# Kernel tuning notes

Hardware: AMD Instinct MI355X
Metric: run time of the kernel (lower is better)

The kernel has to match this reference:

```python
import jax, jax.numpy as jnp
import numpy as np

N_HID = 4
EPS = 1e-6  # LayerNorm eps (note: added to std, torch-style, std with ddof=1)


def _rnn_layer(wx_out, prev_pre, uh, g, b):
    """Sequential recurrence: at = wx_out[k] + h @ Uh^T; skip-subtract prev pre-act;
    custom layernorm (gamma*(x-mean)/(std+eps)+beta, std unbiased); relu.
    Returns (hiddens [T,B,H], pre_acts [T,B,H])."""
    T, B, H = wx_out.shape

    def step(h, inp):
        wx_k, prev_k = inp
        at = wx_k + h @ uh.T          # [B,H]
        pre = at
        a = at - prev_k               # skip connection (subtract prev layer pre-act)
        mean = a.mean(-1, keepdims=True)
        std = jnp.std(a, axis=-1, ddof=1, keepdims=True)
        a = g * (a - mean) / (std + EPS) + b
        h_new = jax.nn.relu(a)        # drop_mask = 1-drop_rate = 1.0 (test mode, drop_rate=0)
        return h_new, (h_new, pre)

    h0 = jnp.zeros((B, H), wx_out.dtype)
    _, (hs, pres) = jax.lax.scan(step, h0, (wx_out, prev_pre))
    return hs, pres


def setup_inputs() -> dict:
    key = jax.random.key(0)
    ks = jax.random.split(key, 12)
    T, B, D, H, C = 400, 32, 440, 1024, 3500
    s = 0.02
    return {
        "x": jax.random.normal(ks[0], (T, B, D), dtype=jnp.float32),
        "lab": jax.random.randint(ks[1], (T, B), 0, C),
        "test_flag": 1,
        "wx0_w": jax.random.normal(ks[2], (H, D), dtype=jnp.float32) * s,
        "wx0_b": jnp.zeros((H,), jnp.float32),
        "wx_w": jax.random.normal(ks[3], (N_HID - 1, H, H), dtype=jnp.float32) * s,
        "wx_b": jnp.zeros((N_HID - 1, H), jnp.float32),
        "uh_w": jax.random.normal(ks[4], (N_HID, H, H), dtype=jnp.float32) * s,
        "ln_g": jnp.ones((N_HID, H), jnp.float32),
        "ln_b": jnp.zeros((N_HID, H), jnp.float32),
        "fco_w": jax.random.normal(ks[5], (C, H), dtype=jnp.float32) * s,
        "fco_b": jnp.zeros((C,), jnp.float32),
    }


def reference(x, lab, test_flag, wx0_w, wx0_b, wx_w, wx_b, uh_w, ln_g, ln_b, fco_w, fco_b):
    T, B, _ = x.shape
    H = uh_w.shape[-1]
    prev_pre = jnp.zeros((T, B, H), x.dtype)  # skip_conn: layer 0 subtracts zeros
    h = x
    for i in range(N_HID):
        if i == 0:
            wx_out = jnp.einsum('tbd,hd->tbh', h, wx0_w) + wx0_b
        else:
            wx_out = jnp.einsum('tbd,hd->tbh', h, wx_w[i - 1]) + wx_b[i - 1]
        h, prev_pre = _rnn_layer(wx_out, prev_pre, uh_w[i], ln_g[i], ln_b[i])
    out = jnp.einsum('tbh,ch->tbc', h, fco_w) + fco_b   # [T,B,C]
    pout = jax.nn.log_softmax(out, axis=2)
    pred = jnp.argmax(pout, axis=2)
    nll = -jnp.take_along_axis(pout, lab[..., None], axis=2).squeeze(-1)
    loss = nll.mean()
    err = jnp.mean((pred != lab).astype(jnp.float32))
    return loss, err, pout
```

## Files before the change

kernel.cpp:

```cpp
#include <hip/hip_runtime.h>
#include <math.h>

#define T_STEPS 400
#define BATCH   32
#define HID     1024
#define MROWS   (T_STEPS * BATCH)
#define NCLS    3500
#define NG      8
#define BPG     4
#define CPG     32
#define JS      32
#define EPS     1e-6f
#define SLOTP   8

typedef __attribute__((ext_vector_type(8))) short short8v;
typedef __attribute__((ext_vector_type(4))) float f32x4;

__device__ __forceinline__ unsigned short bf16_rne(float x) {
  unsigned u = __builtin_bit_cast(unsigned, x);
  unsigned r = u + 0x7FFFu + ((u >> 16) & 1u);
  return (unsigned short)(r >> 16);
}

__device__ __forceinline__ unsigned pack_w(float x) {
  unsigned short h = bf16_rne(x);
  float fh = __builtin_bit_cast(float, (unsigned)h << 16);
  unsigned short l = bf16_rne(x - fh);
  return ((unsigned)h << 16) | (unsigned)l;
}
__device__ __forceinline__ float unpk_w(unsigned u) {
  float hi = __builtin_bit_cast(float, u & 0xFFFF0000u);
  float lo = __builtin_bit_cast(float, u << 16);
  return hi + lo;
}

__device__ __forceinline__ void stage_tile(
    const float* __restrict__ src, int rowlim, int row0, int ld,
    int k0, int K, unsigned short* hi, unsigned short* lo, int tid) {
  #pragma unroll
  for (int it = 0; it < 2; ++it) {
    const int task = tid + 256 * it;
    const int r = task >> 2, q = task & 3;
    const int gr = row0 + r;
    const bool rok = gr < rowlim;
    const float* p = src + (size_t)gr * ld + k0 + q * 8;
    float x[8];
    if (rok && (k0 + 32 <= K)) {
      float4 v0 = *(const float4*)p;
      float4 v1 = *(const float4*)(p + 4);
      x[0] = v0.x; x[1] = v0.y; x[2] = v0.z; x[3] = v0.w;
      x[4] = v1.x; x[5] = v1.y; x[6] = v1.z; x[7] = v1.w;
    } else {
      #pragma unroll
      for (int j = 0; j < 8; ++j)
        x[j] = (rok && (k0 + q * 8 + j) < K) ? p[j] : 0.f;
    }
    unsigned hp[4], lp[4];
    #pragma unroll
    for (int j = 0; j < 4; ++j) {
      unsigned short h0 = bf16_rne(x[2 * j]), h1 = bf16_rne(x[2 * j + 1]);
      float f0 = __builtin_bit_cast(float, (unsigned)h0 << 16);
      float f1 = __builtin_bit_cast(float, (unsigned)h1 << 16);
      unsigned short l0 = bf16_rne(x[2 * j] - f0), l1 = bf16_rne(x[2 * j + 1] - f1);
      hp[j] = (unsigned)h0 | ((unsigned)h1 << 16);
      lp[j] = (unsigned)l0 | ((unsigned)l1 << 16);
    }
    const int idx = (r * 4 + (q ^ (r & 3))) * 8;
    *(uint4*)&hi[idx] = make_uint4(hp[0], hp[1], hp[2], hp[3]);
    *(uint4*)&lo[idx] = make_uint4(lp[0], lp[1], lp[2], lp[3]);
  }
}

template <int NPASS>
__global__ __launch_bounds__(256) void gemm_mfma(
    const float* __restrict__ A, const float* __restrict__ W,
    const float* __restrict__ bias, float* __restrict__ C,
    int M, int N, int K) {
  __shared__ unsigned short Ah[128 * 32], Al[128 * 32];
  __shared__ unsigned short Bh[128 * 32], Bl[128 * 32];
  const int tid = threadIdx.x;
  const int m0 = blockIdx.y * 128, n0 = blockIdx.x * 128;
  const int w = tid >> 6, lane = tid & 63;
  const int rlow = lane & 15, ksel = lane >> 4;

  f32x4 acc[8][2];
  #pragma unroll
  for (int i = 0; i < 8; ++i) {
    acc[i][0] = (f32x4)(0.f);
    acc[i][1] = (f32x4)(0.f);
  }

  for (int k0 = 0; k0 < K; k0 += 32) {
    __syncthreads();
    stage_tile(A, M, m0, K, k0, K, Ah, Al, tid);
    stage_tile(W, N, n0, K, k0, K, Bh, Bl, tid);
    __syncthreads();

    short8v wh[2], wl[2];
    #pragma unroll
    for (int nf = 0; nf < 2; ++nf) {
      const int rn = w * 32 + nf * 16 + rlow;
      const int idx = (rn * 4 + (ksel ^ (rn & 3))) * 8;
      wh[nf] = *(const short8v*)&Bh[idx];
      if (NPASS == 3) wl[nf] = *(const short8v*)&Bl[idx];
    }
    #pragma unroll
    for (int i = 0; i < 8; ++i) {
      const int ra = i * 16 + rlow;
      const int idx = (ra * 4 + (ksel ^ (ra & 3))) * 8;
      short8v ah = *(const short8v*)&Ah[idx];
      if (NPASS == 3) {
        short8v al = *(const short8v*)&Al[idx];
        acc[i][0] = __builtin_amdgcn_mfma_f32_16x16x32_bf16(ah, wh[0], acc[i][0], 0, 0, 0);
        acc[i][0] = __builtin_amdgcn_mfma_f32_16x16x32_bf16(al, wh[0], acc[i][0], 0, 0, 0);
        acc[i][0] = __builtin_amdgcn_mfma_f32_16x16x32_bf16(ah, wl[0], acc[i][0], 0, 0, 0);
        acc[i][1] = __builtin_amdgcn_mfma_f32_16x16x32_bf16(ah, wh[1], acc[i][1], 0, 0, 0);
        acc[i][1] = __builtin_amdgcn_mfma_f32_16x16x32_bf16(al, wh[1], acc[i][1], 0, 0, 0);
        acc[i][1] = __builtin_amdgcn_mfma_f32_16x16x32_bf16(ah, wl[1], acc[i][1], 0, 0, 0);
      } else {
        acc[i][0] = __builtin_amdgcn_mfma_f32_16x16x32_bf16(ah, wh[0], acc[i][0], 0, 0, 0);
        acc[i][1] = __builtin_amdgcn_mfma_f32_16x16x32_bf16(ah, wh[1], acc[i][1], 0, 0, 0);
      }
    }
  }

  int col[2]; float bb[2]; bool cok[2];
  #pragma unroll
  for (int nf = 0; nf < 2; ++nf) {
    col[nf] = n0 + w * 32 + nf * 16 + rlow;
    cok[nf] = col[nf] < N;
    bb[nf] = cok[nf] ? bias[col[nf]] : 0.f;
  }
  #pragma unroll
  for (int i = 0; i < 8; ++i) {
    const int row = m0 + i * 16 + ksel * 4;
    #pragma unroll
    for (int nf = 0; nf < 2; ++nf) {
      if (cok[nf]) {
        float* cp = C + (size_t)row * N + col[nf];
        cp[0 * N] = acc[i][nf][0] + bb[nf];
        cp[1 * N] = acc[i][nf][1] + bb[nf];
        cp[2 * N] = acc[i][nf][2] + bb[nf];
        cp[3 * N] = acc[i][nf][3] + bb[nf];
      }
    }
  }
}

__global__ __launch_bounds__(256, 1) void scan_pair(
    const float* __restrict__ wx,
    const float* __restrict__ ua_w,
    const float* __restrict__ ub_w,
    const float* __restrict__ wb_w,
    const float* __restrict__ wb_bias,
    float* __restrict__ h_all,
    float* __restrict__ pre_prev,
    float* __restrict__ pre_out,
    float* __restrict__ a_pub,
    int* __restrict__ prog,
    const float* __restrict__ g_a, const float* __restrict__ be_a,
    const float* __restrict__ g_b, const float* __restrict__ be_b,
    int skip_sub) {
  const int tid  = threadIdx.x;
  const int g    = blockIdx.x >> 5;
  const int c    = blockIdx.x & 31;
  const int lane = tid & 63;
  const int wv   = tid >> 6;
  const int jw   = tid & 3;
  const int ks   = tid >> 2;
  const int col0 = c * JS + jw * 8;

  int* prog_g = prog + (size_t)g * CPG * SLOTP;

  __shared__ float h_a_lds[HID * BPG];
  __shared__ float h_b_lds[HID * BPG];
  __shared__ float a_lds[BPG * HID];
  __shared__ float partial_a[4][BPG][JS];
  __shared__ float partial_b[4][BPG][JS];
  __shared__ float stats_lds[BPG][2];

  float4 ua0[16], ua1[16], ub0[16], ub1[16];
  uint4  wp0[16], wp1[16];
  #pragma unroll
  for (int i = 0; i < 16; ++i) {
    const int kk = ks + 64 * i;
    float a0[8], b0[8], w0[8];
    #pragma unroll
    for (int q = 0; q < 8; ++q) {
      const size_t off = (size_t)(col0 + q) * HID + kk;
      a0[q] = ua_w[off];
      b0[q] = ub_w[off];
      w0[q] = wb_w[off];
    }
    ua0[i] = make_float4(a0[0], a0[1], a0[2], a0[3]);
    ua1[i] = make_float4(a0[4], a0[5], a0[6], a0[7]);
    ub0[i] = make_float4(b0[0], b0[1], b0[2], b0[3]);
    ub1[i] = make_float4(b0[4], b0[5], b0[6], b0[7]);
    wp0[i] = make_uint4(pack_w(w0[0]), pack_w(w0[1]), pack_w(w0[2]), pack_w(w0[3]));
    wp1[i] = make_uint4(pack_w(w0[4]), pack_w(w0[5]), pack_w(w0[6]), pack_w(w0[7]));
  }
  float ga[4], ba[4], gb[4], bb[4];
  #pragma unroll
  for (int j = 0; j < 4; ++j) {
    const int kk = tid + 256 * j;
    ga[j] = g_a[kk]; ba[j] = be_a[kk];
    gb[j] = g_b[kk]; bb[j] = be_b[kk];
  }
  float biasb = 0.f;
  if (tid < 128) biasb = wb_bias[c * JS + (tid & 31)];

  float wxa_r = 0.f, prev_r = 0.f, pre_a_reg = 0.f;
  if (tid < 128) {
    const size_t gi = ((size_t)0 * BATCH + g * BPG + (tid >> 5)) * HID + c * JS + (tid & 31);
    wxa_r = wx[gi];
    if (!skip_sub)
      prev_r = __hip_atomic_load(&pre_prev[gi], __ATOMIC_RELAXED, __HIP_MEMORY_SCOPE_AGENT);
  }
  __syncthreads();

  for (int k = 0; k <= T_STEPS; ++k) {
    const int par = k & 1;
    float* pa = a_pub + ((size_t)(par * 2 + 0) * NG + g) * (BPG * HID);
    float* pb = a_pub + ((size_t)(par * 2 + 1) * NG + g) * (BPG * HID);
    const bool doA = (k < T_STEPS);
    const bool doB = (k >= 1);

    if (doA && k > 0) {
      float pacc[4][8];
      #pragma unroll
      for (int b = 0; b < 4; ++b)
        #pragma unroll
        for (int q = 0; q < 8; ++q) pacc[b][q] = 0.f;
      #pragma unroll
      for (int i = 0; i < 16; ++i) {
        float4 h4 = *(const float4*)&h_a_lds[(ks + 64 * i) * 4];
        #pragma unroll
        for (int b = 0; b < 4; ++b) {
          float hb = ((const float*)&h4)[b];
          pacc[b][0] += hb * ua0[i].x; pacc[b][1] += hb * ua0[i].y;
          pacc[b][2] += hb * ua0[i].z; pacc[b][3] += hb * ua0[i].w;
          pacc[b][4] += hb * ua1[i].x; pacc[b][5] += hb * ua1[i].y;
          pacc[b][6] += hb * ua1[i].z; pacc[b][7] += hb * ua1[i].w;
        }
      }
      #pragma unroll
      for (int b = 0; b < 4; ++b)
        #pragma unroll
        for (int q = 0; q < 8; ++q) {
          float v = pacc[b][q];
          v += __shfl_xor(v, 4); v += __shfl_xor(v, 8);
          v += __shfl_xor(v, 16); v += __shfl_xor(v, 32);
          pacc[b][q] = v;
        }
      if ((lane >> 2) == 0) {
        #pragma unroll
        for (int b = 0; b < 4; ++b) {
          *(float4*)&partial_a[wv][b][jw * 8]     = *(const float4*)&pacc[b][0];
          *(float4*)&partial_a[wv][b][jw * 8 + 4] = *(const float4*)&pacc[b][4];
        }
      }
    }

    if (doB) {
      float pacc[4][8];
      #pragma unroll
      for (int b = 0; b < 4; ++b)
        #pragma unroll
        for (int q = 0; q < 8; ++q) pacc[b][q] = 0.f;
      #pragma unroll
      for (int i = 0; i < 16; ++i) {
        float4 ha = *(const float4*)&h_a_lds[(ks + 64 * i) * 4];
        float w[8];
        w[0] = unpk_w(wp0[i].x); w[1] = unpk_w(wp0[i].y);
        w[2] = unpk_w(wp0[i].z); w[3] = unpk_w(wp0[i].w);
        w[4] = unpk_w(wp1[i].x); w[5] = unpk_w(wp1[i].y);
        w[6] = unpk_w(wp1[i].z); w[7] = unpk_w(wp1[i].w);
        #pragma unroll
        for (int b = 0; b < 4; ++b) {
          float hv = ((const float*)&ha)[b];
          #pragma unroll
          for (int q = 0; q < 8; ++q) pacc[b][q] += hv * w[q];
        }
        if (k >= 2) {
          float4 hb4 = *(const float4*)&h_b_lds[(ks + 64 * i) * 4];
          #pragma unroll
          for (int b = 0; b < 4; ++b) {
            float hv = ((const float*)&hb4)[b];
            pacc[b][0] += hv * ub0[i].x; pacc[b][1] += hv * ub0[i].y;
            pacc[b][2] += hv * ub0[i].z; pacc[b][3] += hv * ub0[i].w;
            pacc[b][4] += hv * ub1[i].x; pacc[b][5] += hv * ub1[i].y;
            pacc[b][6] += hv * ub1[i].z; pacc[b][7] += hv * ub1[i].w;
          }
        }
      }
      #pragma unroll
      for (int b = 0; b < 4; ++b)
        #pragma unroll
        for (int q = 0; q < 8; ++q) {
          float v = pacc[b][q];
          v += __shfl_xor(v, 4); v += __shfl_xor(v, 8);
          v += __shfl_xor(v, 16); v += __shfl_xor(v, 32);
          pacc[b][q] = v;
        }
      if ((lane >> 2) == 0) {
        #pragma unroll
        for (int b = 0; b < 4; ++b) {
          *(float4*)&partial_b[wv][b][jw * 8]     = *(const float4*)&pacc[b][0];
          *(float4*)&partial_b[wv][b][jw * 8 + 4] = *(const float4*)&pacc[b][4];
        }
      }
    }
    __syncthreads();

    if (tid < 128) {
      const int b = tid >> 5, j = tid & 31;
      float at_a_new = 0.f;
      if (doA) {
        float red = 0.f;
        if (k > 0)
          red = partial_a[0][b][j] + partial_a[1][b][j]
              + partial_a[2][b][j] + partial_a[3][b][j];
        at_a_new = wxa_r + red;
        __hip_atomic_store(&pa[(size_t)b * HID + c * JS + j], at_a_new - prev_r,
                           __ATOMIC_RELAXED, __HIP_MEMORY_SCOPE_AGENT);
      }
      if (doB) {
        float redb = partial_b[0][b][j] + partial_b[1][b][j]
                   + partial_b[2][b][j] + partial_b[3][b][j];
        float at_b = biasb + redb;
        const size_t gib = ((size_t)(k - 1) * BATCH + g * BPG + b) * HID + c * JS + j;
        __hip_atomic_store(&pre_out[gib], at_b,
                           __ATOMIC_RELAXED, __HIP_MEMORY_SCOPE_AGENT);
        __hip_atomic_store(&pb[(size_t)b * HID + c * JS + j], at_b - pre_a_reg,
                           __ATOMIC_RELAXED, __HIP_MEMORY_SCOPE_AGENT);
      }
      if (doA) pre_a_reg = at_a_new;
    }
    asm volatile("s_waitcnt vmcnt(0)" ::: "memory");
    __syncthreads();

    if (tid == 0)
      __hip_atomic_store(&prog_g[c * SLOTP], k + 1,
                         __ATOMIC_RELAXED, __HIP_MEMORY_SCOPE_AGENT);

    float wxa_n = 0.f, prev_n = 0.f;
    if (k + 1 < T_STEPS && tid < 128) {
      const size_t gi = ((size_t)(k + 1) * BATCH + g * BPG + (tid >> 5)) * HID
                        + c * JS + (tid & 31);
      wxa_n = wx[gi];
      if (!skip_sub)
        prev_n = __hip_atomic_load(&pre_prev[gi], __ATOMIC_RELAXED, __HIP_MEMORY_SCOPE_AGENT);
    }

    {
      const int* p = &prog_g[(lane & 31) * SLOTP];
      while (true) {
        int v = __hip_atomic_load(p, __ATOMIC_RELAXED, __HIP_MEMORY_SCOPE_AGENT);
        if (__all(v >= k + 1)) break;
        __builtin_amdgcn_s_sleep(1);
      }
    }

    float ta[16], tb[16];
    if (doA) {
      #pragma unroll
      for (int j = 0; j < 16; ++j)
        ta[j] = __hip_atomic_load(&pa[tid + 256 * j],
                                  __ATOMIC_RELAXED, __HIP_MEMORY_SCOPE_AGENT);
    }
    if (doB) {
      #pragma unroll
      for (int j = 0; j < 16; ++j)
        tb[j] = __hip_atomic_load(&pb[tid + 256 * j],
                                  __ATOMIC_RELAXED, __HIP_MEMORY_SCOPE_AGENT);
    }

    if (doA) {
      #pragma unroll
      for (int j = 0; j < 16; ++j) a_lds[tid + 256 * j] = ta[j];
      __syncthreads();
      {
        float s1 = 0.f, s2 = 0.f;
        #pragma unroll
        for (int i = 0; i < 16; ++i) {
          float v = a_lds[wv * HID + i * 64 + lane];
          s1 += v; s2 += v * v;
        }
        #pragma unroll
        for (int m = 1; m <= 32; m <<= 1) { s1 += __shfl_xor(s1, m); s2 += __shfl_xor(s2, m); }
        if (lane == 0) {
          float mean = s1 * (1.f / HID);
          float var = (s2 - (float)HID * mean * mean) * (1.f / (float)(HID - 1));
          stats_lds[wv][0] = mean;
          stats_lds[wv][1] = sqrtf(fmaxf(var, 0.f)) + EPS;
        }
      }
      __syncthreads();
      {
        float m0 = stats_lds[0][0], r0 = 1.f / stats_lds[0][1];
        float m1 = stats_lds[1][0], r1 = 1.f / stats_lds[1][1];
        float m2 = stats_lds[2][0], r2 = 1.f / stats_lds[2][1];
        float m3 = stats_lds[3][0], r3 = 1.f / stats_lds[3][1];
        #pragma unroll
        for (int j = 0; j < 4; ++j) {
          const int kk = tid + 256 * j;
          float h0 = fmaxf(ga[j] * (a_lds[0 * HID + kk] - m0) * r0 + ba[j], 0.f);
          float h1 = fmaxf(ga[j] * (a_lds[1 * HID + kk] - m1) * r1 + ba[j], 0.f);
          float h2 = fmaxf(ga[j] * (a_lds[2 * HID + kk] - m2) * r2 + ba[j], 0.f);
          float h3 = fmaxf(ga[j] * (a_lds[3 * HID + kk] - m3) * r3 + ba[j], 0.f);
          *(float4*)&h_a_lds[kk * 4] = make_float4(h0, h1, h2, h3);
        }
      }
      __syncthreads();
    }

    if (doB) {
      #pragma unroll
      for (int j = 0; j < 16; ++j) a_lds[tid + 256 * j] = tb[j];
      __syncthreads();
      {
        float s1 = 0.f, s2 = 0.f;
        #pragma unroll
        for (int i = 0; i < 16; ++i) {
          float v = a_lds[wv * HID + i * 64 + lane];
          s1 += v; s2 += v * v;
        }
        #pragma unroll
        for (int m = 1; m <= 32; m <<= 1) { s1 += __shfl_xor(s1, m); s2 += __shfl_xor(s2, m); }
        if (lane == 0) {
          float mean = s1 * (1.f / HID);
          float var = (s2 - (float)HID * mean * mean) * (1.f / (float)(HID - 1));
          stats_lds[wv][0] = mean;
          stats_lds[wv][1] = sqrtf(fmaxf(var, 0.f)) + EPS;
        }
      }
      __syncthreads();
      {
        float m0 = stats_lds[0][0], r0 = 1.f / stats_lds[0][1];
        float m1 = stats_lds[1][0], r1 = 1.f / stats_lds[1][1];
        float m2 = stats_lds[2][0], r2 = 1.f / stats_lds[2][1];
        float m3 = stats_lds[3][0], r3 = 1.f / stats_lds[3][1];
        #pragma unroll
        for (int j = 0; j < 4; ++j) {
          const int kk = tid + 256 * j;
          float h0 = fmaxf(gb[j] * (a_lds[0 * HID + kk] - m0) * r0 + bb[j], 0.f);
          float h1 = fmaxf(gb[j] * (a_lds[1 * HID + kk] - m1) * r1 + bb[j], 0.f);
          float h2 = fmaxf(gb[j] * (a_lds[2 * HID + kk] - m2) * r2 + bb[j], 0.f);
          float h3 = fmaxf(gb[j] * (a_lds[3 * HID + kk] - m3) * r3 + bb[j], 0.f);
          *(float4*)&h_b_lds[kk * 4] = make_float4(h0, h1, h2, h3);
          if (c == 0) {
            const size_t hb0 = ((size_t)(k - 1) * BATCH + g * BPG) * HID + kk;
            h_all[hb0 + 0 * HID] = h0;
            h_all[hb0 + 1 * HID] = h1;
            h_all[hb0 + 2 * HID] = h2;
            h_all[hb0 + 3 * HID] = h3;
          }
        }
      }
    }
    __syncthreads();

    wxa_r = wxa_n; prev_r = prev_n;
  }
}

__global__ __launch_bounds__(256) void softmax_loss(
    float* __restrict__ out, const int* __restrict__ lab, float* __restrict__ acc) {
  __shared__ float rowbuf[NCLS];
  __shared__ float rv[4]; __shared__ int ri[4]; __shared__ float rs[4];
  __shared__ float shv[2];
  __shared__ int shidx;
  const int m = blockIdx.x;
  float* row = out + (size_t)m * NCLS;
  const int tid = threadIdx.x;
  const int lane = tid & 63, wid = tid >> 6;

  float vmax = -1e30f; int vidx = 0x7fffffff;
  for (int c2 = tid; c2 < NCLS / 2; c2 += 256) {
    float2 v = *(const float2*)(row + 2 * c2);
    rowbuf[2 * c2] = v.x; rowbuf[2 * c2 + 1] = v.y;
    if (v.x > vmax) { vmax = v.x; vidx = 2 * c2; }
    if (v.y > vmax) { vmax = v.y; vidx = (v.x > v.y) ? vidx : 2 * c2 + 1; }
  }
  #pragma unroll
  for (int off = 32; off; off >>= 1) {
    float ov = __shfl_down(vmax, off);
    int oi = __shfl_down(vidx, off);
    if (ov > vmax || (ov == vmax && oi < vidx)) { vmax = ov; vidx = oi; }
  }
  if (lane == 0) { rv[wid] = vmax; ri[wid] = vidx; }
  __syncthreads();
  if (tid == 0) {
    float bm = rv[0]; int bi = ri[0];
    for (int w = 1; w < 4; ++w)
      if (rv[w] > bm || (rv[w] == bm && ri[w] < bi)) { bm = rv[w]; bi = ri[w]; }
    shv[0] = bm; shidx = bi;
  }
  __syncthreads();
  float gmax = shv[0];
  float s = 0.f;
  for (int c = tid; c < NCLS; c += 256) s += expf(rowbuf[c] - gmax);
  #pragma unroll
  for (int off = 32; off; off >>= 1) s += __shfl_down(s, off);
  if (lane == 0) rs[wid] = s;
  __syncthreads();
  if (tid == 0) shv[1] = rs[0] + rs[1] + rs[2] + rs[3];
  __syncthreads();
  float lse = logf(shv[1]);
  for (int c2 = tid; c2 < NCLS / 2; c2 += 256) {
    float2 v;
    v.x = rowbuf[2 * c2] - gmax - lse;
    v.y = rowbuf[2 * c2 + 1] - gmax - lse;
    *(float2*)(row + 2 * c2) = v;
  }
  if (tid == 0) {
    int lb = lab[m];
    float nll = -(rowbuf[lb] - gmax - lse);
    atomicAdd(acc + 0, nll);
    atomicAdd(acc + 1, (shidx != lb) ? 1.f : 0.f);
  }
}

__global__ void init_acc(float* acc) { acc[threadIdx.x] = 0.f; }

__global__ void finalize_out(const float* __restrict__ acc, float* __restrict__ out) {
  out[0] = acc[0] * (1.f / (float)MROWS);
  out[1] = acc[1] * (1.f / (float)MROWS);
}

extern "C" void kernel_launch(void* const* d_in, const int* in_sizes, int n_in,
                              void* d_out, int out_size, void* d_ws, size_t ws_size,
                              hipStream_t stream) {
  const float* x     = (const float*)d_in[0];
  const int*   lab   = (const int*)d_in[1];
  const float* wx0_w = (const float*)d_in[3];
  const float* wx0_b = (const float*)d_in[4];
  const float* wx_w  = (const float*)d_in[5];
  const float* wx_b  = (const float*)d_in[6];
  const float* uh_w  = (const float*)d_in[7];
  const float* ln_g  = (const float*)d_in[8];
  const float* ln_b  = (const float*)d_in[9];
  const float* fco_w = (const float*)d_in[10];
  const float* fco_b = (const float*)d_in[11];
  float* out = (float*)d_out;

  float* wsf = (float*)d_ws;
  size_t off = 0;
  auto carve = [&](size_t n) { float* p = wsf + off; off += (n + 63) & ~(size_t)63; return p; };
  float* wxbuf = carve((size_t)MROWS * HID);
  float* h_all = carve((size_t)MROWS * HID);
  float* pre   = carve((size_t)MROWS * HID);
  float* a_pub = carve((size_t)2 * 2 * NG * BPG * HID);
  int*   prog  = (int*)carve((size_t)2 * NG * CPG * SLOTP);
  float* acc   = carve(64);

  (void)hipMemsetAsync(prog, 0, (size_t)2 * NG * CPG * SLOTP * sizeof(int), stream);
  init_acc<<<1, 2, 0, stream>>>(acc);

  const size_t HH = (size_t)HID * HID;

  gemm_mfma<3><<<dim3(HID / 128, MROWS / 128), 256, 0, stream>>>(
      x, wx0_w, wx0_b, wxbuf, MROWS, HID, 440);
  scan_pair<<<dim3(NG * CPG), 256, 0, stream>>>(
      wxbuf, uh_w + 0 * HH, uh_w + 1 * HH, wx_w + 0 * HH, wx_b + 0 * HID,
      h_all, pre , pre, a_pub, prog,
      ln_g + 0 * HID, ln_b + 0 * HID, ln_g + 1 * HID, ln_b + 1 * HID, 1);

  gemm_mfma<3><<<dim3(HID / 128, MROWS / 128), 256, 0, stream>>>(
      h_all, wx_w + 1 * HH, wx_b + 1 * HID, wxbuf, MROWS, HID, HID);
  scan_pair<<<dim3(NG * CPG), 256, 0, stream>>>(
      wxbuf, uh_w + 2 * HH, uh_w + 3 * HH, wx_w + 2 * HH, wx_b + 2 * HID,
      h_all, pre , pre, a_pub, prog + (size_t)NG * CPG * SLOTP,
      ln_g + 2 * HID, ln_b + 2 * HID, ln_g + 3 * HID, ln_b + 3 * HID, 0);

  gemm_mfma<1><<<dim3((NCLS + 127) / 128, MROWS / 128), 256, 0, stream>>>(
      h_all, fco_w, fco_b, out + 2, MROWS, NCLS, HID);
  softmax_loss<<<MROWS, 256, 0, stream>>>(out + 2, lab, acc);
  finalize_out<<<1, 1, 0, stream>>>(acc, out);
}
```

Measured before the change: 11.08 ms.

## Double scan block threads and process both layer normalizations concurrently

Raises the persistent scan kernel from 256 to 512 threads per block, splitting each K-reduction over 8 waves with 8 slices per thread. This frees enough registers to hold the inter-layer weight in plain fp32 instead of packed bf16 hi/lo pairs. It also merges the two per-step layernorm phases (layer A and layer B) into one pass where each half of the block handles one layer, which removes several barriers per timestep. The cost is more partial sums to reduce across waves, a larger shared-memory footprint, and a layout change to the published activation buffer.

Result: slower. 16.52 ms (+49.0%).

```diff
diff --git a/kernel.cpp b/kernel.cpp
--- a/kernel.cpp
+++ b/kernel.cpp
@@ -20,18 +20,6 @@
   unsigned u = __builtin_bit_cast(unsigned, x);
   unsigned r = u + 0x7FFFu + ((u >> 16) & 1u);
   return (unsigned short)(r >> 16);
-}
-
-__device__ __forceinline__ unsigned pack_w(float x) {
-  unsigned short h = bf16_rne(x);
-  float fh = __builtin_bit_cast(float, (unsigned)h << 16);
-  unsigned short l = bf16_rne(x - fh);
-  return ((unsigned)h << 16) | (unsigned)l;
-}
-__device__ __forceinline__ float unpk_w(unsigned u) {
-  float hi = __builtin_bit_cast(float, u & 0xFFFF0000u);
-  float lo = __builtin_bit_cast(float, u << 16);
-  return hi + lo;
 }
 
 __device__ __forceinline__ void stage_tile(
@@ -147,7 +135,7 @@
   }
 }
 
-__global__ __launch_bounds__(256, 1) void scan_pair(
+__global__ __launch_bounds__(512, 1) void scan_pair(
     const float* __restrict__ wx,
     const float* __restrict__ ua_w,
     const float* __restrict__ ub_w,
@@ -174,16 +162,15 @@
 
   __shared__ float h_a_lds[HID * BPG];
   __shared__ float h_b_lds[HID * BPG];
-  __shared__ float a_lds[BPG * HID];
-  __shared__ float partial_a[4][BPG][JS];
-  __shared__ float partial_b[4][BPG][JS];
-  __shared__ float stats_lds[BPG][2];
-
-  float4 ua0[16], ua1[16], ub0[16], ub1[16];
-  uint4  wp0[16], wp1[16];
-  #pragma unroll
-  for (int i = 0; i < 16; ++i) {
-    const int kk = ks + 64 * i;
+  __shared__ float a2_lds[2 * BPG * HID];
+  __shared__ float partial_a[8][BPG][JS];
+  __shared__ float partial_b[8][BPG][JS];
+  __shared__ float stats_lds[8][2];
+
+  float4 ua0[8], ua1[8], ub0[8], ub1[8], wb0[8], wb1[8];
+  #pragma unroll
+  for (int i = 0; i < 8; ++i) {
+    const int kk = ks + 128 * i;
     float a0[8], b0[8], w0[8];
     #pragma unroll
     for (int q = 0; q < 8; ++q) {
@@ -196,15 +183,16 @@
     ua1[i] = make_float4(a0[4], a0[5], a0[6], a0[7]);
     ub0[i] = make_float4(b0[0], b0[1], b0[2], b0[3]);
     ub1[i] = make_float4(b0[4], b0[5], b0[6], b0[7]);
-    wp0[i] = make_uint4(pack_w(w0[0]), pack_w(w0[1]), pack_w(w0[2]), pack_w(w0[3]));
-    wp1[i] = make_uint4(pack_w(w0[4]), pack_w(w0[5]), pack_w(w0[6]), pack_w(w0[7]));
-  }
-  float ga[4], ba[4], gb[4], bb[4];
+    wb0[i] = make_float4(w0[0], w0[1], w0[2], w0[3]);
+    wb1[i] = make_float4(w0[4], w0[5], w0[6], w0[7]);
+  }
+  const int half = tid >> 8, t2 = tid & 255;
+  float gq[4], bq[4];
   #pragma unroll
   for (int j = 0; j < 4; ++j) {
-    const int kk = tid + 256 * j;
-    ga[j] = g_a[kk]; ba[j] = be_a[kk];
-    gb[j] = g_b[kk]; bb[j] = be_b[kk];
+    const int kk = t2 + 256 * j;
+    gq[j] = half ? g_b[kk] : g_a[kk];
+    bq[j] = half ? be_b[kk] : be_a[kk];
   }
   float biasb = 0.f;
   if (tid < 128) biasb = wb_bias[c * JS + (tid & 31)];
@@ -220,8 +208,7 @@
 
   for (int k = 0; k <= T_STEPS; ++k) {
     const int par = k & 1;
-    float* pa = a_pub + ((size_t)(par * 2 + 0) * NG + g) * (BPG * HID);
-    float* pb = a_pub + ((size_t)(par * 2 + 1) * NG + g) * (BPG * HID);
+    float* pbase = a_pub + ((size_t)par * NG + g) * (2 * BPG * HID);
     const bool doA = (k < T_STEPS);
     const bool doB = (k >= 1);
 
@@ -232,8 +219,8 @@
         #pragma unroll
         for (int q = 0; q < 8; ++q) pacc[b][q] = 0.f;
       #pragma unroll
-      for (int i = 0; i < 16; ++i) {
-        float4 h4 = *(const float4*)&h_a_lds[(ks + 64 * i) * 4];
+      for (int i = 0; i < 8; ++i) {
+        float4 h4 = *(const float4*)&h_a_lds[(ks + 128 * i) * 4];
         #pragma unroll
         for (int b = 0; b < 4; ++b) {
           float hb = ((const float*)&h4)[b];
@@ -268,21 +255,18 @@
         #pragma unroll
         for (int q = 0; q < 8; ++q) pacc[b][q] = 0.f;
       #pragma unroll
-      for (int i = 0; i < 16; ++i) {
-        float4 ha = *(const float4*)&h_a_lds[(ks + 64 * i) * 4];
-        float w[8];
-        w[0] = unpk_w(wp0[i].x); w[1] = unpk_w(wp0[i].y);
-        w[2] = unpk_w(wp0[i].z); w[3] = unpk_w(wp0[i].w);
-        w[4] = unpk_w(wp1[i].x); w[5] = unpk_w(wp1[i].y);
-        w[6] = unpk_w(wp1[i].z); w[7] = unpk_w(wp1[i].w);
+      for (int i = 0; i < 8; ++i) {
+        float4 ha = *(const float4*)&h_a_lds[(ks + 128 * i) * 4];
         #pragma unroll
         for (int b = 0; b < 4; ++b) {
           float hv = ((const float*)&ha)[b];
-          #pragma unroll
-          for (int q = 0; q < 8; ++q) pacc[b][q] += hv * w[q];
+          pacc[b][0] += hv * wb0[i].x; pacc[b][1] += hv * wb0[i].y;
+          pacc[b][2] += hv * wb0[i].z; pacc[b][3] += hv * wb0[i].w;
+          pacc[b][4] += hv * wb1[i].x; pacc[b][5] += hv * wb1[i].y;
+          pacc[b][6] += hv * wb1[i].z; pacc[b][7] += hv * wb1[i].w;
         }
         if (k >= 2) {
-          float4 hb4 = *(const float4*)&h_b_lds[(ks + 64 * i) * 4];
+          float4 hb4 = *(const float4*)&h_b_lds[(ks + 128 * i) * 4];
           #pragma unroll
           for (int b = 0; b < 4; ++b) {
             float hv = ((const float*)&hb4)[b];
@@ -317,21 +301,24 @@
       float at_a_new = 0.f;
       if (doA) {
         float red = 0.f;
-        if (k > 0)
-          red = partial_a[0][b][j] + partial_a[1][b][j]
-              + partial_a[2][b][j] + partial_a[3][b][j];
+        if (k > 0) {
+          #pragma unroll
+          for (int w = 0; w < 8; ++w) red += partial_a[w][b][j];
+        }
         at_a_new = wxa_r + red;
-        __hip_atomic_store(&pa[(size_t)b * HID + c * JS + j], at_a_new - prev_r,
+        __hip_atomic_store(&pbase[(size_t)b * HID + c * JS + j], at_a_new - prev_r,
                            __ATOMIC_RELAXED, __HIP_MEMORY_SCOPE_AGENT);
       }
       if (doB) {
-        float redb = partial_b[0][b][j] + partial_b[1][b][j]
-                   + partial_b[2][b][j] + partial_b[3][b][j];
+        float redb = 0.f;
+        #pragma unroll
+        for (int w = 0; w < 8; ++w) redb += partial_b[w][b][j];
         float at_b = biasb + redb;
         const size_t gib = ((size_t)(k - 1) * BATCH + g * BPG + b) * HID + c * JS + j;
         __hip_atomic_store(&pre_out[gib], at_b,
                            __ATOMIC_RELAXED, __HIP_MEMORY_SCOPE_AGENT);
-        __hip_atomic_store(&pb[(size_t)b * HID + c * JS + j], at_b - pre_a_reg,
+        __hip_atomic_store(&pbase[(size_t)(BPG * HID) + b * HID + c * JS + j],
+                           at_b - pre_a_reg,
                            __ATOMIC_RELAXED, __HIP_MEMORY_SCOPE_AGENT);
       }
       if (doA) pre_a_reg = at_a_new;
@@ -361,100 +348,56 @@
       }
     }
 
-    float ta[16], tb[16];
-    if (doA) {
-      #pragma unroll
-      for (int j = 0; j < 16; ++j)
-        ta[j] = __hip_atomic_load(&pa[tid + 256 * j],
-                                  __ATOMIC_RELAXED, __HIP_MEMORY_SCOPE_AGENT);
-    }
-    if (doB) {
-      #pragma unroll
-      for (int j = 0; j < 16; ++j)
-        tb[j] = __hip_atomic_load(&pb[tid + 256 * j],
-                                  __ATOMIC_RELAXED, __HIP_MEMORY_SCOPE_AGENT);
-    }
-
-    if (doA) {
-      #pragma unroll
-      for (int j = 0; j < 16; ++j) a_lds[tid + 256 * j] = ta[j];
-      __syncthreads();
-      {
-        float s1 = 0.f, s2 = 0.f;
-        #pragma unroll
-        for (int i = 0; i < 16; ++i) {
-          float v = a_lds[wv * HID + i * 64 + lane];
-          s1 += v; s2 += v * v;
-        }
-        #pragma unroll
-        for (int m = 1; m <= 32; m <<= 1) { s1 += __shfl_xor(s1, m); s2 += __shfl_xor(s2, m); }
-        if (lane == 0) {
-          float mean = s1 * (1.f / HID);
-          float var = (s2 - (float)HID * mean * mean) * (1.f / (float)(HID - 1));
-          stats_lds[wv][0] = mean;
-          stats_lds[wv][1] = sqrtf(fmaxf(var, 0.f)) + EPS;
-        }
-      }
-      __syncthreads();
-      {
-        float m0 = stats_lds[0][0], r0 = 1.f / stats_lds[0][1];
-        float m1 = stats_lds[1][0], r1 = 1.f / stats_lds[1][1];
-        float m2 = stats_lds[2][0], r2 = 1.f / stats_lds[2][1];
-        float m3 = stats_lds[3][0], r3 = 1.f / stats_lds[3][1];
-        #pragma unroll
-        for (int j = 0; j < 4; ++j) {
-          const int kk = tid + 256 * j;
-          float h0 = fmaxf(ga[j] * (a_lds[0 * HID + kk] - m0) * r0 + ba[j], 0.f);
-          float h1 = fmaxf(ga[j] * (a_lds[1 * HID + kk] - m1) * r1 + ba[j], 0.f);
-          float h2 = fmaxf(ga[j] * (a_lds[2 * HID + kk] - m2) * r2 + ba[j], 0.f);
-          float h3 = fmaxf(ga[j] * (a_lds[3 * HID + kk] - m3) * r3 + ba[j], 0.f);
-          *(float4*)&h_a_lds[kk * 4] = make_float4(h0, h1, h2, h3);
-        }
-      }
-      __syncthreads();
-    }
-
-    if (doB) {
-      #pragma unroll
-      for (int j = 0; j < 16; ++j) a_lds[tid + 256 * j] = tb[j];
-      __syncthreads();
-      {
-        float s1 = 0.f, s2 = 0.f;
-        #pragma unroll
-        for (int i = 0; i < 16; ++i) {
-          float v = a_lds[wv * HID + i * 64 + lane];
-          s1 += v; s2 += v * v;
-        }
-        #pragma unroll
-        for (int m = 1; m <= 32; m <<= 1) { s1 += __shfl_xor(s1, m); s2 += __shfl_xor(s2, m); }
-        if (lane == 0) {
-          float mean = s1 * (1.f / HID);
-          float var = (s2 - (float)HID * mean * mean) * (1.f / (float)(HID - 1));
-          stats_lds[wv][0] = mean;
-          stats_lds[wv][1] = sqrtf(fmaxf(var, 0.f)) + EPS;
-        }
-      }
-      __syncthreads();
-      {
-        float m0 = stats_lds[0][0], r0 = 1.f / stats_lds[0][1];
-        float m1 = stats_lds[1][0], r1 = 1.f / stats_lds[1][1];
-        float m2 = stats_lds[2][0], r2 = 1.f / stats_lds[2][1];
-        float m3 = stats_lds[3][0], r3 = 1.f / stats_lds[3][1];
-        #pragma unroll
-        for (int j = 0; j < 4; ++j) {
-          const int kk = tid + 256 * j;
-          float h0 = fmaxf(gb[j] * (a_lds[0 * HID + kk] - m0) * r0 + bb[j], 0.f);
-          float h1 = fmaxf(gb[j] * (a_lds[1 * HID + kk] - m1) * r1 + bb[j], 0.f);
-          float h2 = fmaxf(gb[j] * (a_lds[2 * HID + kk] - m2) * r2 + bb[j], 0.f);
-          float h3 = fmaxf(gb[j] * (a_lds[3 * HID + kk] - m3) * r3 + bb[j], 0.f);
-          *(float4*)&h_b_lds[kk * 4] = make_float4(h0, h1, h2, h3);
-          if (c == 0) {
-            const size_t hb0 = ((size_t)(k - 1) * BATCH + g * BPG) * HID + kk;
-            h_all[hb0 + 0 * HID] = h0;
-            h_all[hb0 + 1 * HID] = h1;
-            h_all[hb0 + 2 * HID] = h2;
-            h_all[hb0 + 3 * HID] = h3;
-          }
+    {
+      #pragma unroll
+      for (int j = 0; j < 16; ++j) {
+        const int idx = tid + 512 * j;
+        a2_lds[idx] = __hip_atomic_load(&pbase[idx],
+                                        __ATOMIC_RELAXED, __HIP_MEMORY_SCOPE_AGENT);
+      }
+    }
+    __syncthreads();
+
+    {
+      float s1 = 0.f, s2 = 0.f;
+      #pragma unroll
+      for (int i = 0; i < 16; ++i) {
+        float v = a2_lds[wv * HID + i * 64 + lane];
+        s1 += v; s2 += v * v;
+      }
+      #pragma unroll
+      for (int m = 1; m <= 32; m <<= 1) { s1 += __shfl_xor(s1, m); s2 += __shfl_xor(s2, m); }
+      if (lane == 0) {
+        float mean = s1 * (1.f / HID);
+        float var = (s2 - (float)HID * mean * mean) * (1.f / (float)(HID - 1));
+        stats_lds[wv][0] = mean;
+        stats_lds[wv][1] = sqrtf(fmaxf(var, 0.f)) + EPS;
+      }
+    }
+    __syncthreads();
+
+    if ((half == 0 && doA) || (half == 1 && doB)) {
+      const int sbase = half * 4;
+      float m0 = stats_lds[sbase + 0][0], r0 = 1.f / stats_lds[sbase + 0][1];
+      float m1 = stats_lds[sbase + 1][0], r1 = 1.f / stats_lds[sbase + 1][1];
+      float m2 = stats_lds[sbase + 2][0], r2 = 1.f / stats_lds[sbase + 2][1];
+      float m3 = stats_lds[sbase + 3][0], r3 = 1.f / stats_lds[sbase + 3][1];
+      const int abase = half * (BPG * HID);
+      float* hdst = half ? h_b_lds : h_a_lds;
+      #pragma unroll
+      for (int j = 0; j < 4; ++j) {
+        const int kk = t2 + 256 * j;
+        float h0 = fmaxf(gq[j] * (a2_lds[abase + 0 * HID + kk] - m0) * r0 + bq[j], 0.f);
+        float h1 = fmaxf(gq[j] * (a2_lds[abase + 1 * HID + kk] - m1) * r1 + bq[j], 0.f);
+        float h2 = fmaxf(gq[j] * (a2_lds[abase + 2 * HID + kk] - m2) * r2 + bq[j], 0.f);
+        float h3 = fmaxf(gq[j] * (a2_lds[abase + 3 * HID + kk] - m3) * r3 + bq[j], 0.f);
+        *(float4*)&hdst[kk * 4] = make_float4(h0, h1, h2, h3);
+        if (half == 1 && c == 0) {
+          const size_t hb0 = ((size_t)(k - 1) * BATCH + g * BPG) * HID + kk;
+          h_all[hb0 + 0 * HID] = h0;
+          h_all[hb0 + 1 * HID] = h1;
+          h_all[hb0 + 2 * HID] = h2;
+          h_all[hb0 + 3 * HID] = h3;
         }
       }
     }
@@ -550,7 +493,7 @@
   float* wxbuf = carve((size_t)MROWS * HID);
   float* h_all = carve((size_t)MROWS * HID);
   float* pre   = carve((size_t)MROWS * HID);
-  float* a_pub = carve((size_t)2 * 2 * NG * BPG * HID);
+  float* a_pub = carve((size_t)2 * NG * 2 * BPG * HID);
   int*   prog  = (int*)carve((size_t)2 * NG * CPG * SLOTP);
   float* acc   = carve(64);
 
@@ -561,14 +504,14 @@
 
   gemm_mfma<3><<<dim3(HID / 128, MROWS / 128), 256, 0, stream>>>(
       x, wx0_w, wx0_b, wxbuf, MROWS, HID, 440);
-  scan_pair<<<dim3(NG * CPG), 256, 0, stream>>>(
+  scan_pair<<<dim3(NG * CPG), 512, 0, stream>>>(
       wxbuf, uh_w + 0 * HH, uh_w + 1 * HH, wx_w + 0 * HH, wx_b + 0 * HID,
       h_all, pre , pre, a_pub, prog,
       ln_g + 0 * HID, ln_b + 0 * HID, ln_g + 1 * HID, ln_b + 1 * HID, 1);
 
   gemm_mfma<3><<<dim3(HID / 128, MROWS / 128), 256, 0, stream>>>(
       h_all, wx_w + 1 * HH, wx_b + 1 * HID, wxbuf, MROWS, HID, HID);
-  scan_pair<<<dim3(NG * CPG), 256, 0, stream>>>(
+  scan_pair<<<dim3(NG * CPG), 512, 0, stream>>>(
       wxbuf, uh_w + 2 * HH, uh_w + 3 * HH, wx_w + 2 * HH, wx_b + 2 * HID,
       h_all, pre , pre, a_pub, prog + (size_t)NG * CPG * SLOTP,
       ln_g + 2 * HID, ln_b + 2 * HID, ln_g + 3 * HID, ln_b + 3 * HID, 0);
```
